# Kernel optimization log

Hardware: AMD Instinct MI355X
Metric: run time of the kernel (lower is better)

Reference implementation:

```python
import jax, jax.numpy as jnp
import numpy as np
import math

N_ENT, N_USR, N_EDGE, C = 100000, 50000, 1000000, 64
N_FACT, N_REL, N_HOPS = 4, 10, 2
KG_HEADS = 2
TEMP = 0.2


def scatter_softmax(scores, seg, num_segments):
    m = jax.ops.segment_max(scores, seg, num_segments=num_segments)
    e = jnp.exp(scores - m[seg])
    s = jax.ops.segment_sum(e, seg, num_segments=num_segments)
    return e / (s[seg] + 1e-16)


def l2norm(x, eps=1e-12):
    n = jnp.linalg.norm(x, axis=-1, keepdims=True)
    return x / jnp.maximum(n, eps)


def setup_inputs() -> dict:
    key = jax.random.key(0)
    ks = jax.random.split(key, 12)
    return {
        "user_emb": jax.random.normal(ks[0], (N_USR, C), jnp.float32) * 0.1,
        "entity_emb": jax.random.normal(ks[1], (N_ENT, C), jnp.float32) * 0.1,
        "latent_emb": jax.random.normal(ks[2], (N_FACT, C), jnp.float32) * 0.1,
        "weight": jax.random.normal(ks[3], (N_REL - 1, C), jnp.float32) * 0.1,
        "disen_weight_att": jax.random.normal(ks[4], (N_FACT, N_REL - 1), jnp.float32) * 0.1,
        "kg_W_r": jax.random.normal(ks[5], (C, C), jnp.float32) * 0.1,
        "ui_vals": jax.random.uniform(ks[6], (N_EDGE,), jnp.float32),
        "edge_index": jax.random.randint(ks[7], (2, N_EDGE), 0, N_ENT, jnp.int64 if jax.config.read('jax_enable_x64') else jnp.int32),
        "edge_type": jax.random.randint(ks[8], (N_EDGE,), 1, N_REL, jnp.int32),
        "ui_rows": jax.random.randint(ks[9], (N_EDGE,), 0, N_USR, jnp.int32),
        "ui_cols": jax.random.randint(ks[10], (N_EDGE,), 0, N_ENT, jnp.int32),
    }


def reference(user_emb, entity_emb, latent_emb, weight, disen_weight_att,
              kg_W_r, ui_vals, edge_index, edge_type, ui_rows, ui_cols):
    head, tail = edge_index[0], edge_index[1]
    d_k = C // KG_HEADS

    # ---- _cul_cor with ind == 'mi' ----
    disen_T = disen_weight_att.T  # [R-1, F]
    nT = disen_T / jnp.linalg.norm(disen_T, axis=1, keepdims=True)
    pos = jnp.sum(nT * nT, axis=1)
    ttl = jnp.sum(disen_T @ disen_weight_att, axis=1)
    cor = -jnp.sum(jnp.log(jnp.exp(pos / TEMP) / jnp.exp(ttl / TEMP)))

    # ---- Invariant_Capture (g_mask=None) ----
    rel_emb = weight[edge_type - 1]          # [E, C]
    head_emb = entity_emb[head]              # [E, C]
    q = (head_emb @ kg_W_r).reshape(-1, KG_HEADS, d_k)
    k = (rel_emb @ kg_W_r).reshape(-1, KG_HEADS, d_k)
    score_r = ((q * k).sum(-1) / math.sqrt(d_k)).mean(-1)  # [E]
    rel_scores = scatter_softmax(score_r, head, N_ENT)
    t_emb = entity_emb[tail]
    r_emb = rel_emb * rel_scores[:, None]
    # bmm of concat(h,r) with concat(t,r) == h.t + r.r
    score_trip = (head_emb * t_emb).sum(-1) + (r_emb * r_emb).sum(-1)
    kg_mask = scatter_softmax(score_trip, head, N_ENT)  # invariant_mask [E]

    # ---- conv_compute: n_hops Aggregator layers, no dropout (eval-determinism) ----
    counts = jnp.clip(jax.ops.segment_sum(jnp.ones_like(kg_mask), head,
                                          num_segments=N_ENT), 1.0)
    disen_w = jax.nn.softmax(disen_weight_att, axis=-1) @ weight  # [F, C]

    ent, usr = entity_emb, user_emb
    ent_res, usr_res = entity_emb, user_emb
    for _ in range(N_HOPS):
        # KG aggregate: scatter_mean over head of masked tail*relation messages
        neigh = ent[tail] * weight[edge_type - 1] * kg_mask[:, None]  # [E, C]
        ent_agg = jax.ops.segment_sum(neigh, head, num_segments=N_ENT) / counts[:, None]
        # user->factor attention on current user embedding
        score = jax.nn.softmax(usr @ latent_emb.T, axis=1)[:, :, None]  # [U, F, 1]
        # sparse user aggregation: interact_mat @ ent
        u_agg = jax.ops.segment_sum(ent[ui_cols] * ui_vals[:, None], ui_rows,
                                    num_segments=N_USR)
        mix = (disen_w[None, :, :] * score).sum(axis=1)  # [U, C]
        u_agg = u_agg * mix + u_agg
        ent = l2norm(ent_agg)
        usr = l2norm(u_agg)
        ent_res = ent_res + ent
        usr_res = usr_res + usr
    return ent_res, usr_res, cor
```

## Files before the change

kernel.cpp:

```cpp
#include <hip/hip_runtime.h>
#include <math.h>

#define N_ENT 100000
#define N_USR 50000
#define N_EDGE 1000000
#define B9 (N_ENT * 9)
#define TEMPC 0.2f
#define KG_BLOCKS (N_ENT / 4)
#define UI_BLOCKS (N_USR / 4)

#define TB_BLOCKS 6250
#define CNT_BLOCKS 489
#define SC_BLOCKS 196
#define REL2_BLOCKS 391

#define BIN_BLOCKS 245
#define NCK 391
#define NCU 196
#define FINEK_BLOCKS NCK
#define FINEU_BLOCKS NCU

#define WLS 68

typedef unsigned short ushort_t;

__device__ __forceinline__ float waveReduceSum(float x) {
#pragma unroll
  for (int d = 32; d > 0; d >>= 1) x += __shfl_xor(x, d);
  return x;
}
__device__ __forceinline__ float waveReduceMax(float x) {
#pragma unroll
  for (int d = 32; d > 0; d >>= 1) x = fmaxf(x, __shfl_xor(x, d));
  return x;
}
__device__ __forceinline__ int waveReduceSumI(int x) {
#pragma unroll
  for (int d = 32; d > 0; d >>= 1) x += __shfl_xor(x, d);
  return x;
}
__device__ __forceinline__ float bf2f(unsigned int u16) {
  union { unsigned int i; float f; } v;
  v.i = u16 << 16;
  return v.f;
}
__device__ __forceinline__ ushort_t f2bf(float f) {
  union { unsigned int i; float f; } v;
  v.f = f;
  unsigned int u = v.i;
  u = (u + 0x7FFFu + ((u >> 16) & 1u)) >> 16;
  return (ushort_t)u;
}
__device__ __forceinline__ int rl(int v, int l) { return __builtin_amdgcn_readlane(v, l); }
__device__ __forceinline__ float rlf(float v, int l) {
  return __int_as_float(__builtin_amdgcn_readlane(__float_as_int(v), l));
}

__device__ __forceinline__ float colRT(float a0, float a1, float a2, float a3,
                                       float a4, float a5, float a6, float a7,
                                       int g, int part) {
#define RED3(x) x += __shfl_xor(x, 8); x += __shfl_xor(x, 16); x += __shfl_xor(x, 32);
  RED3(a0) RED3(a1) RED3(a2) RED3(a3) RED3(a4) RED3(a5) RED3(a6) RED3(a7)
#undef RED3
  float t0 = __shfl(a0, g), t1 = __shfl(a1, g), t2 = __shfl(a2, g), t3 = __shfl(a3, g);
  float t4 = __shfl(a4, g), t5 = __shfl(a5, g), t6 = __shfl(a6, g), t7 = __shfl(a7, g);
  float r = t0;
  r = (part == 1) ? t1 : r;
  r = (part == 2) ? t2 : r;
  r = (part == 3) ? t3 : r;
  r = (part == 4) ? t4 : r;
  r = (part == 5) ? t5 : r;
  r = (part == 6) ? t6 : r;
  r = (part == 7) ? t7 : r;
  return r;
}

__global__ void k_pre(const float* __restrict__ ent0, ushort_t* __restrict__ ent0bf,
                      const int* __restrict__ head, const int* __restrict__ uir,
                      const int* __restrict__ etype,
                      int* __restrict__ cnt_u, int* __restrict__ cnt9,
                      const float* __restrict__ weight, const float* __restrict__ kgW,
                      const float* __restrict__ disen,
                      float* __restrict__ V, float* __restrict__ wsq,
                      float* __restrict__ dw, float* __restrict__ cor_out,
                      const float* __restrict__ user_emb, const float* __restrict__ latent,
                      float4* __restrict__ sc4a) {
  int bid = blockIdx.x;
  if (bid < TB_BLOCKS) {
    int i = bid * 256 + threadIdx.x;
    if (i < N_ENT * 16) {
      float4 v = ((const float4*)ent0)[i];
      ushort4 o;
      o.x = f2bf(v.x); o.y = f2bf(v.y); o.z = f2bf(v.z); o.w = f2bf(v.w);
      ((ushort4*)ent0bf)[i] = o;
    }
  } else if (bid < TB_BLOCKS + CNT_BLOCKS) {
    int i0 = ((bid - TB_BLOCKS) * 256 + threadIdx.x) * 8;
    if (i0 < N_EDGE) {
      int4 ha = *(const int4*)(head + i0), hb = *(const int4*)(head + i0 + 4);
      int4 ea = *(const int4*)(etype + i0), eb = *(const int4*)(etype + i0 + 4);
      int4 ua = *(const int4*)(uir + i0), ub = *(const int4*)(uir + i0 + 4);
      atomicAdd(&cnt9[ha.x * 9 + (ea.x - 1)], 1);
      atomicAdd(&cnt9[ha.y * 9 + (ea.y - 1)], 1);
      atomicAdd(&cnt9[ha.z * 9 + (ea.z - 1)], 1);
      atomicAdd(&cnt9[ha.w * 9 + (ea.w - 1)], 1);
      atomicAdd(&cnt9[hb.x * 9 + (eb.x - 1)], 1);
      atomicAdd(&cnt9[hb.y * 9 + (eb.y - 1)], 1);
      atomicAdd(&cnt9[hb.z * 9 + (eb.z - 1)], 1);
      atomicAdd(&cnt9[hb.w * 9 + (eb.w - 1)], 1);
      atomicAdd(&cnt_u[ua.x], 1);
      atomicAdd(&cnt_u[ua.y], 1);
      atomicAdd(&cnt_u[ua.z], 1);
      atomicAdd(&cnt_u[ua.w], 1);
      atomicAdd(&cnt_u[ub.x], 1);
      atomicAdd(&cnt_u[ub.y], 1);
      atomicAdd(&cnt_u[ub.z], 1);
      atomicAdd(&cnt_u[ub.w], 1);
    }
  } else if (bid == TB_BLOCKS + CNT_BLOCKS) {
    __shared__ float T[9 * 64];
    __shared__ float sm[4 * 9];
    int tid = threadIdx.x;
    for (int e = tid; e < 9 * 64; e += 256) {
      int r = e >> 6, d = e & 63;
      float s = 0.f;
      for (int k = 0; k < 64; ++k) s += kgW[k * 64 + d] * weight[r * 64 + k];
      T[e] = s;
    }
    if (tid < 4) {
      float m = -INFINITY;
      for (int r = 0; r < 9; ++r) m = fmaxf(m, disen[tid * 9 + r]);
      float den = 0.f;
      float ex[9];
      for (int r = 0; r < 9; ++r) { ex[r] = expf(disen[tid * 9 + r] - m); den += ex[r]; }
      for (int r = 0; r < 9; ++r) sm[tid * 9 + r] = ex[r] / den;
    }
    __syncthreads();
    for (int e = tid; e < 9 * 64; e += 256) {
      int r = e >> 6, i = e & 63;
      float s = 0.f;
      for (int d = 0; d < 64; ++d) s += kgW[i * 64 + d] * T[r * 64 + d];
      V[e] = s;
    }
    if (tid < 9) {
      float s = 0.f;
      for (int c = 0; c < 64; ++c) { float w = weight[tid * 64 + c]; s += w * w; }
      wsq[tid] = s;
    }
    for (int e = tid; e < 4 * 64; e += 256) {
      int f = e >> 6, c = e & 63;
      float s = 0.f;
      for (int r = 0; r < 9; ++r) s += sm[f * 9 + r] * weight[r * 64 + c];
      dw[e] = s;
    }
    if (tid == 0) {
      float rowsum[4];
      for (int f = 0; f < 4; ++f) {
        float s = 0.f;
        for (int j = 0; j < 9; ++j) s += disen[f * 9 + j];
        rowsum[f] = s;
      }
      float cor = 0.f;
      for (int i = 0; i < 9; ++i) {
        float n2 = 0.f, ttl = 0.f;
        for (int f = 0; f < 4; ++f) {
          float v = disen[f * 9 + i];
          n2 += v * v;
          ttl += v * rowsum[f];
        }
        float nrm = sqrtf(n2);
        float pos = 0.f;
        for (int f = 0; f < 4; ++f) {
          float v = disen[f * 9 + i] / nrm;
          pos += v * v;
        }
        cor += (ttl - pos) / TEMPC;
      }
      *cor_out = cor;
    }
  } else {
    __shared__ __align__(16) float lat[256];
    if (threadIdx.x < 256) lat[threadIdx.x] = latent[threadIdx.x];
    __syncthreads();
    int u = (bid - TB_BLOCKS - CNT_BLOCKS - 1) * 256 + threadIdx.x;
    if (u >= N_USR) return;
    float a0 = 0.f, a1 = 0.f, a2 = 0.f, a3 = 0.f;
    const float4* row = (const float4*)(user_emb + (size_t)u * 64);
#pragma unroll
    for (int q = 0; q < 16; ++q) {
      float4 v = row[q];
      float4 l0 = *(const float4*)(lat + 0 * 64 + q * 4);
      float4 l1 = *(const float4*)(lat + 1 * 64 + q * 4);
      float4 l2 = *(const float4*)(lat + 2 * 64 + q * 4);
      float4 l3 = *(const float4*)(lat + 3 * 64 + q * 4);
      a0 = fmaf(v.x, l0.x, a0); a0 = fmaf(v.y, l0.y, a0); a0 = fmaf(v.z, l0.z, a0); a0 = fmaf(v.w, l0.w, a0);
      a1 = fmaf(v.x, l1.x, a1); a1 = fmaf(v.y, l1.y, a1); a1 = fmaf(v.z, l1.z, a1); a1 = fmaf(v.w, l1.w, a1);
      a2 = fmaf(v.x, l2.x, a2); a2 = fmaf(v.y, l2.y, a2); a2 = fmaf(v.z, l2.z, a2); a2 = fmaf(v.w, l2.w, a2);
      a3 = fmaf(v.x, l3.x, a3); a3 = fmaf(v.y, l3.y, a3); a3 = fmaf(v.z, l3.z, a3); a3 = fmaf(v.w, l3.w, a3);
    }
    sc4a[u] = make_float4(a0, a1, a2, a3);
  }
}

__global__ void k_scanred(const int* __restrict__ cnt9, const int* __restrict__ cnt_u,
                          int* __restrict__ bsum_h, int* __restrict__ bsum_u, int nbh) {
  int b = blockIdx.x, tid = threadIdx.x;
  int s = 0;
  if (b < nbh) {
    int i0 = b * 1024 + tid * 4;
#pragma unroll
    for (int k = 0; k < 4; ++k)
      if (i0 + k < B9) s += cnt9[i0 + k];
  } else {
    int i0 = (b - nbh) * 1024 + tid * 4;
#pragma unroll
    for (int k = 0; k < 4; ++k)
      if (i0 + k < N_USR) s += cnt_u[i0 + k];
  }
  s = waveReduceSumI(s);
  __shared__ int l[4];
  int lane = tid & 63, wid = tid >> 6;
  if (lane == 0) l[wid] = s;
  __syncthreads();
  if (tid == 0) {
    int v = l[0] + l[1] + l[2] + l[3];
    if (b < nbh) bsum_h[b] = v; else bsum_u[b - nbh] = v;
  }
}

__global__ void __launch_bounds__(1024) k_scan_tops(
    int* bsA, int nA, int* bsB, int nB,
    int* ptrA, int NA, int* ptrB, int NB, int total) {
  __shared__ int wsum[16];
  int tid = threadIdx.x, lane = tid & 63, wid = tid >> 6;
  int v = (tid < nA) ? bsA[tid] : 0;
  int x = v;
#pragma unroll
  for (int d = 1; d < 64; d <<= 1) {
    int y = __shfl_up(x, d);
    if (lane >= d) x += y;
  }
  if (lane == 63) wsum[wid] = x;
  __syncthreads();
  if (tid == 0) {
    int a = 0;
    for (int w = 0; w < 16; ++w) { int t = wsum[w]; wsum[w] = a; a += t; }
  }
  __syncthreads();
  if (tid < nA) bsA[tid] = x - v + wsum[wid];
  if (tid == 0) ptrA[NA] = total;
  __syncthreads();
  int vb = (tid < nB) ? bsB[tid] : 0;
  int xb = vb;
#pragma unroll
  for (int d = 1; d < 64; d <<= 1) {
    int y = __shfl_up(xb, d);
    if (lane >= d) xb += y;
  }
  if (lane == 63) wsum[wid] = xb;
  __syncthreads();
  if (tid == 0) {
    int a = 0;
    for (int w = 0; w < 16; ++w) { int t = wsum[w]; wsum[w] = a; a += t; }
  }
  __syncthreads();
  if (tid < nB) bsB[tid] = xb - vb + wsum[wid];
  if (tid == 0) ptrB[NB] = total;
}

__global__ void k_scanfin(const int* __restrict__ cnt9, const int* __restrict__ cnt_u,
                          const int* __restrict__ bsum_h, const int* __restrict__ bsum_u,
                          int* __restrict__ base9, int* __restrict__ head_ptr,
                          int* __restrict__ ui_ptr,
                          int* __restrict__ coarse_kg_cur, int* __restrict__ coarse_ui_cur,
                          int nbh) {
  int b = blockIdx.x, tid = threadIdx.x;
  bool isH = (b < nbh);
  int bl = isH ? b : b - nbh;
  int n = isH ? B9 : N_USR;
  int i0 = bl * 1024 + tid * 4;
  int s = 0;
  int loc[4];
#pragma unroll
  for (int k = 0; k < 4; ++k) {
    int v = 0;
    if (i0 + k < n) v = isH ? cnt9[i0 + k] : cnt_u[i0 + k];
    loc[k] = s;
    s += v;
  }
  int lane = tid & 63, wid = tid >> 6;
  int x = s;
#pragma unroll
  for (int d = 1; d < 64; d <<= 1) {
    int y = __shfl_up(x, d);
    if (lane >= d) x += y;
  }
  __shared__ int l[4];
  if (lane == 63) l[wid] = x;
  __syncthreads();
  if (tid == 0) {
    int a = 0;
    for (int w = 0; w < 4; ++w) { int t = l[w]; l[w] = a; a += t; }
  }
  __syncthreads();
  int excl = x - s + l[wid] + (isH ? bsum_h[bl] : bsum_u[bl]);
#pragma unroll
  for (int k = 0; k < 4; ++k) {
    int idx = i0 + k;
    if (idx < n) {
      int v = excl + loc[k];
      if (isH) {
        base9[idx] = v;
        int ent = idx / 9;
        if (idx - ent * 9 == 0) {
          head_ptr[ent] = v;
          if ((ent & 255) == 0) coarse_kg_cur[ent >> 8] = v;
        }
      } else {
        ui_ptr[idx] = v;
        if ((idx & 255) == 0) coarse_ui_cur[idx >> 8] = v;
      }
    }
  }
}

__global__ void __launch_bounds__(1024) k_bin(
    const int* __restrict__ head, const int* __restrict__ tail,
    const int* __restrict__ etype,
    const int* __restrict__ uir, const int* __restrict__ uic,
    const float* __restrict__ uival,
    int* __restrict__ coarse_kg_cur, int* __restrict__ coarse_ui_cur,
    unsigned int* __restrict__ stage_kg, int2* __restrict__ stage_ui) {
  __shared__ int histK[NCK], histU[NCU];
  int tid = threadIdx.x;
  for (int i = tid; i < NCK; i += 1024) histK[i] = 0;
  for (int i = tid; i < NCU; i += 1024) histU[i] = 0;
  __syncthreads();
  int i0 = (blockIdx.x * 1024 + tid) * 4;
  bool valid = (i0 < N_EDGE);
  int4 h4, t4v, e4, r4, c4;
  float4 v4;
  int k0 = 0, k1 = 0, k2 = 0, k3 = 0, u0 = 0, u1 = 0, u2 = 0, u3 = 0;
  if (valid) {
    h4 = *(const int4*)(head + i0);
    t4v = *(const int4*)(tail + i0);
    e4 = *(const int4*)(etype + i0);
    r4 = *(const int4*)(uir + i0);
    c4 = *(const int4*)(uic + i0);
    v4 = *(const float4*)(uival + i0);
    k0 = atomicAdd(&histK[h4.x >> 8], 1);
    k1 = atomicAdd(&histK[h4.y >> 8], 1);
    k2 = atomicAdd(&histK[h4.z >> 8], 1);
    k3 = atomicAdd(&histK[h4.w >> 8], 1);
    u0 = atomicAdd(&histU[r4.x >> 8], 1);
    u1 = atomicAdd(&histU[r4.y >> 8], 1);
    u2 = atomicAdd(&histU[r4.z >> 8], 1);
    u3 = atomicAdd(&histU[r4.w >> 8], 1);
  }
  __syncthreads();
  if (tid < NCK) {
    int c = histK[tid];
    histK[tid] = (c > 0) ? atomicAdd(&coarse_kg_cur[tid], c) : 0;
  } else if (tid >= 512 && tid < 512 + NCU) {
    int bu = tid - 512;
    int c = histU[bu];
    histU[bu] = (c > 0) ? atomicAdd(&coarse_ui_cur[bu], c) : 0;
  }
  __syncthreads();
  if (valid) {
    stage_kg[histK[h4.x >> 8] + k0] =
        (unsigned int)(t4v.x | ((e4.x - 1) << 20) | ((h4.x & 255) << 24));
    stage_kg[histK[h4.y >> 8] + k1] =
        (unsigned int)(t4v.y | ((e4.y - 1) << 20) | ((h4.y & 255) << 24));
    stage_kg[histK[h4.z >> 8] + k2] =
        (unsigned int)(t4v.z | ((e4.z - 1) << 20) | ((h4.z & 255) << 24));
    stage_kg[histK[h4.w >> 8] + k3] =
        (unsigned int)(t4v.w | ((e4.w - 1) << 20) | ((h4.w & 255) << 24));
    stage_ui[histU[r4.x >> 8] + u0] = make_int2(c4.x | ((r4.x & 255) << 24), __float_as_int(v4.x));
    stage_ui[histU[r4.y >> 8] + u1] = make_int2(c4.y | ((r4.y & 255) << 24), __float_as_int(v4.y));
    stage_ui[histU[r4.z >> 8] + u2] = make_int2(c4.z | ((r4.z & 255) << 24), __float_as_int(v4.z));
    stage_ui[histU[r4.w >> 8] + u3] = make_int2(c4.w | ((r4.w & 255) << 24), __float_as_int(v4.w));
  }
}

__global__ void k_fine_rel2(const unsigned int* __restrict__ stage_kg,
                            const int2* __restrict__ stage_ui,
                            const int* __restrict__ base9, const int* __restrict__ ui_ptr,
                            int* __restrict__ packed, int2* __restrict__ cv,
                            const ushort_t* __restrict__ ent0bf, const float* __restrict__ V,
                            const float* __restrict__ wsq, const int* __restrict__ cnt9,
                            float* __restrict__ rel2t) {
  int tid = threadIdx.x;
  if (blockIdx.x < FINEK_BLOCKS) {
    int b = blockIdx.x;
    __shared__ int lbase[2304];
    __shared__ int lcnt[2304];
    int gb = (b << 8) * 9;
    for (int i = tid; i < 2304; i += 256) {
      int gi = gb + i;
      lbase[i] = (gi < B9) ? base9[gi] : N_EDGE;
      lcnt[i] = 0;
    }
    __syncthreads();
    int start = base9[gb];
    int end = (b < FINEK_BLOCKS - 1) ? base9[gb + 2304] : N_EDGE;
    for (int i = start + tid; i < end; i += 256) {
      unsigned int w = stage_kg[i];
      int key = (int)((w >> 24) & 255u) * 9 + (int)((w >> 20) & 15u);
      int r = atomicAdd(&lcnt[key], 1);
      packed[lbase[key] + r] = (int)(w & 0xFFFFFFu);
    }
  } else if (blockIdx.x < FINEK_BLOCKS + FINEU_BLOCKS) {
    int b = blockIdx.x - FINEK_BLOCKS;
    __shared__ int lbu[256];
    __shared__ int lcu[256];
    int gb = b << 8;
    lbu[tid] = (gb + tid < N_USR) ? ui_ptr[gb + tid] : N_EDGE;
    lcu[tid] = 0;
    __syncthreads();
    int start = ui_ptr[gb];
    int nxt = gb + 256;
    int end = ui_ptr[(nxt < N_USR) ? nxt : N_USR];
    for (int i = start + tid; i < end; i += 256) {
      int2 d = stage_ui[i];
      int key = (d.x >> 24) & 255;
      int r = atomicAdd(&lcu[key], 1);
      cv[lbu[key] + r] = make_int2(d.x & 0xFFFFFF, d.y);
    }
  } else {
    __shared__ __align__(16) float Vl[576];
    __shared__ float wsql[9];
    for (int i = tid; i < 576; i += 256) Vl[i] = V[i];
    if (tid < 9) wsql[tid] = wsq[tid];
    __syncthreads();
    int ent = (blockIdx.x - FINEK_BLOCKS - FINEU_BLOCKS) * 256 + tid;
    if (ent >= N_ENT) return;
    float a[9] = {0, 0, 0, 0, 0, 0, 0, 0, 0};
    const uint4* row = (const uint4*)(ent0bf + (ent << 6));
#pragma unroll
    for (int q = 0; q < 8; ++q) {
      uint4 b = row[q];
      float ch0 = bf2f(b.x & 0xFFFFu), ch1 = bf2f(b.x >> 16);
      float ch2 = bf2f(b.y & 0xFFFFu), ch3 = bf2f(b.y >> 16);
      float ch4 = bf2f(b.z & 0xFFFFu), ch5 = bf2f(b.z >> 16);
      float ch6 = bf2f(b.w & 0xFFFFu), ch7 = bf2f(b.w >> 16);
#pragma unroll
      for (int r = 0; r < 9; ++r) {
        const float4* vp = (const float4*)(Vl + r * 64 + q * 8);
        float4 v0 = vp[0], v1 = vp[1];
        float t = a[r];
        t = fmaf(ch0, v0.x, t); t = fmaf(ch1, v0.y, t);
        t = fmaf(ch2, v0.z, t); t = fmaf(ch3, v0.w, t);
        t = fmaf(ch4, v1.x, t); t = fmaf(ch5, v1.y, t);
        t = fmaf(ch6, v1.z, t); t = fmaf(ch7, v1.w, t);
        a[r] = t;
      }
    }
    const float inv2s = 0.08838834764831845f;
    int cnt[9];
#pragma unroll
    for (int r = 0; r < 9; ++r) cnt[r] = cnt9[ent * 9 + r];
    float m1 = -INFINITY;
#pragma unroll
    for (int r = 0; r < 9; ++r)
      if (cnt[r] > 0) m1 = fmaxf(m1, a[r] * inv2s);
    if (m1 == -INFINITY) {
#pragma unroll
      for (int r = 0; r < 9; ++r) rel2t[ent * 9 + r] = 0.f;
      return;
    }
    float den1 = 1e-16f;
#pragma unroll
    for (int r = 0; r < 9; ++r)
      if (cnt[r] > 0) den1 += (float)cnt[r] * expf(a[r] * inv2s - m1);
#pragma unroll
    for (int r = 0; r < 9; ++r) {
      float rs = expf(a[r] * inv2s - m1) / den1;
      rel2t[ent * 9 + r] = rs * rs * wsql[r];
    }
  }
}

__device__ __forceinline__ float kg_agg64(int deg, int lane, int pk, float mk,
                                          const ushort_t* __restrict__ srcbf,
                                          const float* __restrict__ wl) {
  float a0 = 0.f, a1 = 0.f, a2 = 0.f, a3 = 0.f;
  int j = 0;
  for (; j + 4 <= deg; j += 4) {
    int p0 = rl(pk, j), p1 = rl(pk, j + 1), p2 = rl(pk, j + 2), p3 = rl(pk, j + 3);
    float k0 = rlf(mk, j), k1 = rlf(mk, j + 1), k2 = rlf(mk, j + 2), k3 = rlf(mk, j + 3);
    float r0 = bf2f(srcbf[((p0 & 0xFFFFF) << 6) + lane]);
    float r1 = bf2f(srcbf[((p1 & 0xFFFFF) << 6) + lane]);
    float r2 = bf2f(srcbf[((p2 & 0xFFFFF) << 6) + lane]);
    float r3 = bf2f(srcbf[((p3 & 0xFFFFF) << 6) + lane]);
    a0 = fmaf(r0 * wl[((p0 >> 20) & 15) * WLS + lane], k0, a0);
    a1 = fmaf(r1 * wl[((p1 >> 20) & 15) * WLS + lane], k1, a1);
    a2 = fmaf(r2 * wl[((p2 >> 20) & 15) * WLS + lane], k2, a2);
    a3 = fmaf(r3 * wl[((p3 >> 20) & 15) * WLS + lane], k3, a3);
  }
  for (; j < deg; ++j) {
    int pj = rl(pk, j);
    float kj = rlf(mk, j);
    a0 = fmaf(bf2f(srcbf[((pj & 0xFFFFF) << 6) + lane]) * wl[((pj >> 20) & 15) * WLS + lane], kj, a0);
  }
  return (a0 + a1) + (a2 + a3);
}

__device__ __forceinline__ void ui_body(int usr, int lane,
                                        const ushort_t* __restrict__ srcbf,
                                        const float4* __restrict__ sc4,
                                        const float* __restrict__ addb,
                                        float* __restrict__ outp, float* __restrict__ nxt,
                                        const int* __restrict__ uptr,
                                        const int2* __restrict__ cv,
                                        const float* __restrict__ dwl,
                                        const float* __restrict__ latl,
                                        float4* __restrict__ sc4out) {
  float4 s4 = sc4[usr];
  float m = fmaxf(fmaxf(s4.x, s4.y), fmaxf(s4.z, s4.w));
  float e0 = expf(s4.x - m), e1 = expf(s4.y - m), e2 = expf(s4.z - m), e3 = expf(s4.w - m);
  float den = e0 + e1 + e2 + e3;
  float mix = (e0 * dwl[lane] + e1 * dwl[64 + lane] + e2 * dwl[128 + lane] + e3 * dwl[192 + lane]) / den;
  int s = uptr[usr], e = uptr[usr + 1];
  int g = lane >> 3, part = lane & 7;
  float a0 = 0.f, a1 = 0.f, a2 = 0.f, a3 = 0.f;
  float a4 = 0.f, a5 = 0.f, a6 = 0.f, a7 = 0.f;
  for (int base = s; base < e; base += 64) {
    int c = min(64, e - base);
    int2 cvl = (lane < c) ? cv[base + lane] : make_int2(0, 0);
    int cl = cvl.x;
    float vl = __int_as_float(cvl.y);
    int nch = (c + 7) >> 3;
#pragma unroll
    for (int cc = 0; cc < 8; ++cc) {
      if (cc < nch) {
        int j = (cc << 3) + g;
        int cj = __shfl(cl, j);
        float vj = __shfl(vl, j);
        uint4 b = *((const uint4*)(srcbf + ((size_t)cj << 6)) + part);
        a0 = fmaf(bf2f(b.x & 0xFFFFu), vj, a0);
        a1 = fmaf(bf2f(b.x >> 16), vj, a1);
        a2 = fmaf(bf2f(b.y & 0xFFFFu), vj, a2);
        a3 = fmaf(bf2f(b.y >> 16), vj, a3);
        a4 = fmaf(bf2f(b.z & 0xFFFFu), vj, a4);
        a5 = fmaf(bf2f(b.z >> 16), vj, a5);
        a6 = fmaf(bf2f(b.w & 0xFFFFu), vj, a6);
        a7 = fmaf(bf2f(b.w >> 16), vj, a7);
      }
    }
  }
  float acc = colRT(a0, a1, a2, a3, a4, a5, a6, a7, g, part);
  float ua = acc * mix + acc;
  float nrm = sqrtf(waveReduceSum(ua * ua));
  float val = ua / fmaxf(nrm, 1e-12f);
  size_t o = (size_t)usr * 64 + lane;
  if (nxt) nxt[o] = val;
  outp[o] = addb[o] + val;
  if (sc4out) {
    float s0 = waveReduceSum(val * latl[lane]);
    float s1 = waveReduceSum(val * latl[64 + lane]);
    float s2 = waveReduceSum(val * latl[128 + lane]);
    float s3 = waveReduceSum(val * latl[192 + lane]);
    if (lane == 0) sc4out[usr] = make_float4(s0, s1, s2, s3);
  }
}

__global__ void k_mask_kg_ui(const float* __restrict__ ent0,
                             const ushort_t* __restrict__ ent0bf,
                             const int* __restrict__ hptr, const int* __restrict__ packed,
                             const float* __restrict__ rel2t,
                             float* __restrict__ mask_s, const float* __restrict__ weight,
                             float* __restrict__ out_ent, ushort_t* __restrict__ ent1bf,
                             const float4* __restrict__ sc4,
                             float* __restrict__ out_usr,
                             float* __restrict__ usr1, const int* __restrict__ uptr,
                             const int2* __restrict__ cv,
                             const float* __restrict__ user_emb, const float* __restrict__ dw,
                             const float* __restrict__ latent, float4* __restrict__ sc4b) {
  int lane = threadIdx.x & 63, wid = threadIdx.x >> 6;
  if (blockIdx.x < KG_BLOCKS) {
    __shared__ __align__(16) float sh_eh[4][64];
    __shared__ __align__(16) float wl[9 * WLS];
    for (int i = threadIdx.x; i < 576; i += 256) wl[(i >> 6) * WLS + (i & 63)] = weight[i];
    int ent = blockIdx.x * 4 + wid;
    int s = hptr[ent], e = hptr[ent + 1];
    float eh = ent0[(size_t)ent * 64 + lane];
    sh_eh[wid][lane] = eh;
    __syncthreads();
    size_t o = (size_t)ent * 64 + lane;
    int deg = e - s;
    if (deg == 0) {
      ent1bf[o] = f2bf(0.f);
      out_ent[o] = eh;
      return;
    }
    if (deg <= 64) {
      int pk = (lane < deg) ? packed[s + lane] : 0;
      int tb = (pk >> 20) & 15;
      float r2sel = rel2t[ent * 9 + ((lane < deg) ? tb : 0)];
      int g = lane >> 3, part = lane & 7;
      const float4* ehq = (const float4*)(sh_eh[wid] + (part << 3));
      float4 ef0 = ehq[0], ef1 = ehq[1];
      int nch = (deg + 7) >> 3;
      float den = 0.f;
      float acc0 = 0.f, acc1 = 0.f, acc2 = 0.f, acc3 = 0.f;
      float acc4 = 0.f, acc5 = 0.f, acc6 = 0.f, acc7 = 0.f;
      float ws8[8];
#pragma unroll
      for (int cc = 0; cc < 8; ++cc) {
        ws8[cc] = 0.f;
        if (cc < nch) {
          int j = (cc << 3) + g;
          int pkj = __shfl(pk, j);
          uint4 b = *((const uint4*)(ent0bf + ((size_t)(pkj & 0xFFFFF) << 6)) + part);
          float r0 = bf2f(b.x & 0xFFFFu), r1 = bf2f(b.x >> 16);
          float r2 = bf2f(b.y & 0xFFFFu), r3 = bf2f(b.y >> 16);
          float r4 = bf2f(b.z & 0xFFFFu), r5 = bf2f(b.z >> 16);
          float r6 = bf2f(b.w & 0xFFFFu), r7 = bf2f(b.w >> 16);
          float s0 = r0 * ef0.x, s1 = r2 * ef0.z, s2 = r4 * ef1.x, s3 = r6 * ef1.z;
          s0 = fmaf(r1, ef0.y, s0); s1 = fmaf(r3, ef0.w, s1);
          s2 = fmaf(r5, ef1.y, s2); s3 = fmaf(r7, ef1.w, s3);
          float sv = (s0 + s1) + (s2 + s3);
          sv += __shfl_xor(sv, 1);
          sv += __shfl_xor(sv, 2);
          sv += __shfl_xor(sv, 4);
          float r2j = __shfl(r2sel, j);
          float w = (j < deg) ? expf(sv + r2j) : 0.f;
          ws8[cc] = w;
          den += w;
          const float4* wp = (const float4*)(wl + ((pkj >> 20) & 15) * WLS + (part << 3));
          float4 w0 = wp[0], w1 = wp[1];
// ... 29 lines not shown
    } else {
      float m2l = -INFINITY;
      for (int base = s; base < e; base += 64) {
        int c = min(64, e - base);
        int pk = (lane < c) ? packed[base + lane] : 0;
        int tb = (pk >> 20) & 15;
        float r2 = rel2t[ent * 9 + ((lane < c) ? tb : 0)];
        int tl = pk & 0xFFFFF;
        const uint4* row = (const uint4*)(ent0bf + (tl << 6));
        const float* ehp = sh_eh[wid];
        float d = 0.f;
#pragma unroll
        for (int q = 0; q < 8; ++q) {
          uint4 a = row[q];
          d += bf2f(a.x & 0xFFFF) * ehp[q * 8 + 0] + bf2f(a.x >> 16) * ehp[q * 8 + 1];
          d += bf2f(a.y & 0xFFFF) * ehp[q * 8 + 2] + bf2f(a.y >> 16) * ehp[q * 8 + 3];
          d += bf2f(a.z & 0xFFFF) * ehp[q * 8 + 4] + bf2f(a.z >> 16) * ehp[q * 8 + 5];
          d += bf2f(a.w & 0xFFFF) * ehp[q * 8 + 6] + bf2f(a.w >> 16) * ehp[q * 8 + 7];
        }
        float trip = d + r2;
        if (lane < c) {
          mask_s[base + lane] = trip;
          m2l = fmaxf(m2l, trip);
        }
      }
      float m2 = waveReduceMax(m2l);
      float denl = 0.f;
      for (int base = s; base < e; base += 64) {
        int c = min(64, e - base);
        denl += (lane < c) ? expf(mask_s[base + lane] - m2) : 0.f;
      }
      float den2 = waveReduceSum(denl) + 1e-16f;
      float acc = 0.f;
      for (int base = s; base < e; base += 64) {
        int c = min(64, e - base);
        int pk = (lane < c) ? packed[base + lane] : 0;
        float mk = 0.f;
        if (lane < c) {
          mk = expf(mask_s[base + lane] - m2) / den2;
          mask_s[base + lane] = mk;
        }
        acc += kg_agg64(c, lane, pk, mk, ent0bf, wl);
      }
      float agg = acc / (float)deg;
      float nrm = sqrtf(waveReduceSum(agg * agg));
      float val = agg / fmaxf(nrm, 1e-12f);
      ent1bf[o] = f2bf(val);
      out_ent[o] = eh + val;
    }
  } else {
    __shared__ float dwl[256];
    __shared__ float latl[256];
    if (threadIdx.x < 256) {
      dwl[threadIdx.x] = dw[threadIdx.x];
      latl[threadIdx.x] = latent[threadIdx.x];
    }
    __syncthreads();
    int usr = (blockIdx.x - KG_BLOCKS) * 4 + wid;
    ui_body(usr, lane, ent0bf, sc4, user_emb, out_usr, usr1,
            uptr, cv, dwl, latl, sc4b);
  }
}

__global__ void k_hop2(const ushort_t* __restrict__ srcbf,
                       float* __restrict__ out_ent,
                       const int* __restrict__ hptr, const int* __restrict__ packed,
                       const float* __restrict__ mask_s, const float* __restrict__ weight,
                       const float* __restrict__ usr1, float* __restrict__ out_usr,
                       const int* __restrict__ uptr, const int2* __restrict__ cv,
                       const float4* __restrict__ sc4,
                       const float* __restrict__ dw) {
  int lane = threadIdx.x & 63, wid = threadIdx.x >> 6;
  if (blockIdx.x < KG_BLOCKS) {
    __shared__ __align__(16) float wl[9 * WLS];
    for (int i = threadIdx.x; i < 576; i += 256) wl[(i >> 6) * WLS + (i & 63)] = weight[i];
    __syncthreads();
    int ent = blockIdx.x * 4 + wid;
    int s = hptr[ent], e = hptr[ent + 1];
    int g = lane >> 3, part = lane & 7;
    float a0 = 0.f, a1 = 0.f, a2 = 0.f, a3 = 0.f;
    float a4 = 0.f, a5 = 0.f, a6 = 0.f, a7 = 0.f;
    for (int base = s; base < e; base += 64) {
      int c = min(64, e - base);
      int pk = (lane < c) ? packed[base + lane] : 0;
      float mk = (lane < c) ? mask_s[base + lane] : 0.f;
      int nch = (c + 7) >> 3;
#pragma unroll
      for (int cc = 0; cc < 8; ++cc) {
        if (cc < nch) {
          int j = (cc << 3) + g;
          int pkj = __shfl(pk, j);
          float mkj = __shfl(mk, j);
          uint4 b = *((const uint4*)(srcbf + ((size_t)(pkj & 0xFFFFF) << 6)) + part);
          float r0 = bf2f(b.x & 0xFFFFu), r1 = bf2f(b.x >> 16);
          float r2 = bf2f(b.y & 0xFFFFu), r3 = bf2f(b.y >> 16);
          float r4 = bf2f(b.z & 0xFFFFu), r5 = bf2f(b.z >> 16);
          float r6 = bf2f(b.w & 0xFFFFu), r7 = bf2f(b.w >> 16);
          const float4* wp = (const float4*)(wl + ((pkj >> 20) & 15) * WLS + (part << 3));
          float4 w0 = wp[0], w1 = wp[1];
          a0 = fmaf(mkj * r0, w0.x, a0);
          a1 = fmaf(mkj * r1, w0.y, a1);
          a2 = fmaf(mkj * r2, w0.z, a2);
          a3 = fmaf(mkj * r3, w0.w, a3);
          a4 = fmaf(mkj * r4, w1.x, a4);
          a5 = fmaf(mkj * r5, w1.y, a5);
          a6 = fmaf(mkj * r6, w1.z, a6);
          a7 = fmaf(mkj * r7, w1.w, a7);
        }
      }
    }
    float aggv = colRT(a0, a1, a2, a3, a4, a5, a6, a7, g, part);
    float n = (float)(e - s);
    float agg = aggv / fmaxf(n, 1.0f);
    float nrm = sqrtf(waveReduceSum(agg * agg));
    float val = agg / fmaxf(nrm, 1e-12f);
    size_t o = (size_t)ent * 64 + lane;
    out_ent[o] = out_ent[o] + val;
  } else {
    __shared__ float dwl[256];
    if (threadIdx.x < 256) dwl[threadIdx.x] = dw[threadIdx.x];
    __syncthreads();
    int usr = (blockIdx.x - KG_BLOCKS) * 4 + wid;
    ui_body(usr, lane, srcbf, sc4, out_usr, out_usr, nullptr,
            uptr, cv, dwl, nullptr, nullptr);
  }
}

extern "C" void kernel_launch(void* const* d_in, const int* in_sizes, int n_in,
                              void* d_out, int out_size, void* d_ws, size_t ws_size,
                              hipStream_t stream) {
  const float* user_emb = (const float*)d_in[0];
  const float* entity_emb = (const float*)d_in[1];
  const float* latent = (const float*)d_in[2];
  const float* weight = (const float*)d_in[3];
  const float* disen = (const float*)d_in[4];
  const float* kgW = (const float*)d_in[5];
  const float* ui_vals = (const float*)d_in[6];
  const int* edge_index = (const int*)d_in[7];
  const int* edge_type = (const int*)d_in[8];
  const int* ui_rows = (const int*)d_in[9];
  const int* ui_cols = (const int*)d_in[10];
  const int* head = edge_index;
  const int* tail = edge_index + N_EDGE;

  char* ws = (char*)d_ws;
  size_t o = 0;
  auto alloc = [&](size_t bytes) -> char* {
    char* p = ws + o;
    o += (bytes + 255) & ~(size_t)255;
    return p;
  };
  int* head_ptr = (int*)alloc((N_ENT + 1) * 4);
  int* ui_ptr = (int*)alloc((N_USR + 1) * 4);
  int* cnt_u = (int*)alloc((size_t)N_USR * 4);
  int* bsum_h = (int*)alloc(1024 * 4);
  int* bsum_u = (int*)alloc(64 * 4);
  int* packed = (int*)alloc((size_t)N_EDGE * 4);
  int2* cv = (int2*)alloc((size_t)N_EDGE * 8);
  float* mask_s = (float*)alloc((size_t)N_EDGE * 4);
  ushort_t* ent0bf = (ushort_t*)alloc((size_t)N_ENT * 64 * 2);
  ushort_t* ent1bf = (ushort_t*)alloc((size_t)N_ENT * 64 * 2);
  float* usr1 = (float*)alloc((size_t)N_USR * 64 * 4);
  int* cnt9 = (int*)alloc((size_t)B9 * 4);
  int* base9 = (int*)alloc((size_t)B9 * 4);
  unsigned int* stage_kg = (unsigned int*)alloc((size_t)N_EDGE * 4);
  int2* stage_ui = (int2*)alloc((size_t)N_EDGE * 8);
  int* coarse_kg_cur = (int*)alloc(NCK * 4);
  int* coarse_ui_cur = (int*)alloc(NCU * 4);
  float* rel2t = (float*)alloc((size_t)N_ENT * 9 * 4);
  float4* sc4a = (float4*)alloc((size_t)N_USR * 16);
  float4* sc4b = (float4*)alloc((size_t)N_USR * 16);
  float* V = (float*)alloc(9 * 64 * 4);
  float* wsq = (float*)alloc(16 * 4);
  float* dw = (float*)alloc(4 * 64 * 4);
  if (o > ws_size) return;

  float* out_ent = (float*)d_out;
  float* out_usr = out_ent + (size_t)N_ENT * 64;
  float* out_cor = out_ent + (size_t)N_ENT * 64 + (size_t)N_USR * 64;

  hipMemsetAsync(cnt_u, 0, (size_t)N_USR * 4, stream);
  hipMemsetAsync(cnt9, 0, (size_t)B9 * 4, stream);

  k_pre<<<TB_BLOCKS + CNT_BLOCKS + 1 + SC_BLOCKS, 256, 0, stream>>>(
      entity_emb, ent0bf, head, ui_rows, edge_type, cnt_u, cnt9,
      weight, kgW, disen, V, wsq, dw, out_cor, user_emb, latent, sc4a);

  int nbh = (B9 + 1023) / 1024;
  int nbu = (N_USR + 1023) / 1024;
  k_scanred<<<nbh + nbu, 256, 0, stream>>>(cnt9, cnt_u, bsum_h, bsum_u, nbh);
  k_scan_tops<<<1, 1024, 0, stream>>>(bsum_h, nbh, bsum_u, nbu, head_ptr, N_ENT, ui_ptr, N_USR, N_EDGE);
  k_scanfin<<<nbh + nbu, 256, 0, stream>>>(cnt9, cnt_u, bsum_h, bsum_u,
                                           base9, head_ptr, ui_ptr,
                                           coarse_kg_cur, coarse_ui_cur, nbh);
  k_bin<<<BIN_BLOCKS, 1024, 0, stream>>>(
      head, tail, edge_type, ui_rows, ui_cols, ui_vals,
      coarse_kg_cur, coarse_ui_cur, stage_kg, stage_ui);
  k_fine_rel2<<<FINEK_BLOCKS + FINEU_BLOCKS + REL2_BLOCKS, 256, 0, stream>>>(
      stage_kg, stage_ui, base9, ui_ptr, packed, cv,
      ent0bf, V, wsq, cnt9, rel2t);

  k_mask_kg_ui<<<KG_BLOCKS + UI_BLOCKS, 256, 0, stream>>>(
      entity_emb, ent0bf, head_ptr, packed, rel2t, mask_s, weight,
      out_ent, ent1bf, sc4a, out_usr, usr1, ui_ptr, cv, user_emb, dw, latent, sc4b);

  k_hop2<<<KG_BLOCKS + UI_BLOCKS, 256, 0, stream>>>(
      ent1bf, out_ent, head_ptr, packed, mask_s, weight,
      usr1, out_usr, ui_ptr, cv, sc4b, dw);
}
```

Baseline: 478.4 us.

## Replace fine-grained global counting and scan with coarse shared-memory histograms

Edge counting now builds per-block shared-memory histograms over coarse 256-entity or 256-user buckets and flushes them with a few global atomics, replacing 16 global atomics per thread into large per-(entity,relation) and per-user count arrays. The three-kernel multi-level scan becomes a single small coarse scan. Fine per-entity/relation offsets are now derived inside the fine binning blocks with a local counting pass and block scan, and the rel2 softmax computation is folded into those blocks using the local counts. This removes large memsets, global atomic traffic and two launches, at the cost of reading the staged edges twice in the fine pass.

```diff
diff --git a/kernel.cpp b/kernel.cpp
--- a/kernel.cpp
+++ b/kernel.cpp
@@ -4,7 +4,6 @@
 #define N_ENT 100000
 #define N_USR 50000
 #define N_EDGE 1000000
-#define B9 (N_ENT * 9)
 #define TEMPC 0.2f
 #define KG_BLOCKS (N_ENT / 4)
 #define UI_BLOCKS (N_USR / 4)
@@ -12,7 +11,6 @@
 #define TB_BLOCKS 6250
 #define CNT_BLOCKS 489
 #define SC_BLOCKS 196
-#define REL2_BLOCKS 391
 
 #define BIN_BLOCKS 245
 #define NCK 391
@@ -77,8 +75,7 @@
 
 __global__ void k_pre(const float* __restrict__ ent0, ushort_t* __restrict__ ent0bf,
                       const int* __restrict__ head, const int* __restrict__ uir,
-                      const int* __restrict__ etype,
-                      int* __restrict__ cnt_u, int* __restrict__ cnt9,
+                      int* __restrict__ ccnt_kg, int* __restrict__ ccnt_ui,
                       const float* __restrict__ weight, const float* __restrict__ kgW,
                       const float* __restrict__ disen,
                       float* __restrict__ V, float* __restrict__ wsq,
@@ -95,28 +92,37 @@
       ((ushort4*)ent0bf)[i] = o;
     }
   } else if (bid < TB_BLOCKS + CNT_BLOCKS) {
-    int i0 = ((bid - TB_BLOCKS) * 256 + threadIdx.x) * 8;
+    __shared__ int histK[NCK], histU[NCU];
+    int tid = threadIdx.x;
+    for (int i = tid; i < NCK; i += 256) histK[i] = 0;
+    for (int i = tid; i < NCU; i += 256) histU[i] = 0;
+    __syncthreads();
+    int i0 = ((bid - TB_BLOCKS) * 256 + tid) * 8;
     if (i0 < N_EDGE) {
       int4 ha = *(const int4*)(head + i0), hb = *(const int4*)(head + i0 + 4);
-      int4 ea = *(const int4*)(etype + i0), eb = *(const int4*)(etype + i0 + 4);
       int4 ua = *(const int4*)(uir + i0), ub = *(const int4*)(uir + i0 + 4);
-      atomicAdd(&cnt9[ha.x * 9 + (ea.x - 1)], 1);
-      atomicAdd(&cnt9[ha.y * 9 + (ea.y - 1)], 1);
-      atomicAdd(&cnt9[ha.z * 9 + (ea.z - 1)], 1);
-      atomicAdd(&cnt9[ha.w * 9 + (ea.w - 1)], 1);
-      atomicAdd(&cnt9[hb.x * 9 + (eb.x - 1)], 1);
-      atomicAdd(&cnt9[hb.y * 9 + (eb.y - 1)], 1);
-      atomicAdd(&cnt9[hb.z * 9 + (eb.z - 1)], 1);
-      atomicAdd(&cnt9[hb.w * 9 + (eb.w - 1)], 1);
-      atomicAdd(&cnt_u[ua.x], 1);
-      atomicAdd(&cnt_u[ua.y], 1);
-      atomicAdd(&cnt_u[ua.z], 1);
-      atomicAdd(&cnt_u[ua.w], 1);
-      atomicAdd(&cnt_u[ub.x], 1);
-      atomicAdd(&cnt_u[ub.y], 1);
-      atomicAdd(&cnt_u[ub.z], 1);
-      atomicAdd(&cnt_u[ub.w], 1);
-    }
+      atomicAdd(&histK[ha.x >> 8], 1);
+      atomicAdd(&histK[ha.y >> 8], 1);
+      atomicAdd(&histK[ha.z >> 8], 1);
+      atomicAdd(&histK[ha.w >> 8], 1);
+      atomicAdd(&histK[hb.x >> 8], 1);
+      atomicAdd(&histK[hb.y >> 8], 1);
+      atomicAdd(&histK[hb.z >> 8], 1);
+      atomicAdd(&histK[hb.w >> 8], 1);
+      atomicAdd(&histU[ua.x >> 8], 1);
+      atomicAdd(&histU[ua.y >> 8], 1);
+      atomicAdd(&histU[ua.z >> 8], 1);
+      atomicAdd(&histU[ua.w >> 8], 1);
+      atomicAdd(&histU[ub.x >> 8], 1);
+      atomicAdd(&histU[ub.y >> 8], 1);
+      atomicAdd(&histU[ub.z >> 8], 1);
+      atomicAdd(&histU[ub.w >> 8], 1);
+    }
+    __syncthreads();
+    for (int i = tid; i < NCK; i += 256)
+      if (histK[i] > 0) atomicAdd(&ccnt_kg[i], histK[i]);
+    for (int i = tid; i < NCU; i += 256)
+      if (histU[i] > 0) atomicAdd(&ccnt_ui[i], histU[i]);
   } else if (bid == TB_BLOCKS + CNT_BLOCKS) {
     __shared__ float T[9 * 64];
     __shared__ float sm[4 * 9];
@@ -202,38 +208,14 @@
   }
 }
 
-__global__ void k_scanred(const int* __restrict__ cnt9, const int* __restrict__ cnt_u,
-                          int* __restrict__ bsum_h, int* __restrict__ bsum_u, int nbh) {
-  int b = blockIdx.x, tid = threadIdx.x;
-  int s = 0;
-  if (b < nbh) {
-    int i0 = b * 1024 + tid * 4;
-#pragma unroll
-    for (int k = 0; k < 4; ++k)
-      if (i0 + k < B9) s += cnt9[i0 + k];
-  } else {
-    int i0 = (b - nbh) * 1024 + tid * 4;
-#pragma unroll
-    for (int k = 0; k < 4; ++k)
-      if (i0 + k < N_USR) s += cnt_u[i0 + k];
-  }
-  s = waveReduceSumI(s);
-  __shared__ int l[4];
-  int lane = tid & 63, wid = tid >> 6;
-  if (lane == 0) l[wid] = s;
-  __syncthreads();
-  if (tid == 0) {
-    int v = l[0] + l[1] + l[2] + l[3];
-    if (b < nbh) bsum_h[b] = v; else bsum_u[b - nbh] = v;
-  }
-}
-
-__global__ void __launch_bounds__(1024) k_scan_tops(
-    int* bsA, int nA, int* bsB, int nB,
-    int* ptrA, int NA, int* ptrB, int NB, int total) {
+__global__ void __launch_bounds__(1024) k_scan_coarse(
+    const int* __restrict__ ccnt_kg, const int* __restrict__ ccnt_ui,
+    int* __restrict__ cbase_kg, int* __restrict__ cbase_ui,
+    int* __restrict__ cur_kg, int* __restrict__ cur_ui,
+    int* __restrict__ head_ptr, int* __restrict__ ui_ptr) {
   __shared__ int wsum[16];
   int tid = threadIdx.x, lane = tid & 63, wid = tid >> 6;
-  int v = (tid < nA) ? bsA[tid] : 0;
+  int v = (tid < NCK) ? ccnt_kg[tid] : 0;
   int x = v;
 #pragma unroll
   for (int d = 1; d < 64; d <<= 1) {
@@ -247,81 +229,27 @@
     for (int w = 0; w < 16; ++w) { int t = wsum[w]; wsum[w] = a; a += t; }
   }
   __syncthreads();
-  if (tid < nA) bsA[tid] = x - v + wsum[wid];
-  if (tid == 0) ptrA[NA] = total;
+  int base = x - v + wsum[wid];
+  if (tid < NCK) { cbase_kg[tid] = base; cur_kg[tid] = base; }
+  if (tid == 0) { cbase_kg[NCK] = N_EDGE; head_ptr[N_ENT] = N_EDGE; }
   __syncthreads();
-  int vb = (tid < nB) ? bsB[tid] : 0;
-  int xb = vb;
+  int vu = (tid < NCU) ? ccnt_ui[tid] : 0;
+  int xu = vu;
 #pragma unroll
   for (int d = 1; d < 64; d <<= 1) {
-    int y = __shfl_up(xb, d);
-    if (lane >= d) xb += y;
-  }
-  if (lane == 63) wsum[wid] = xb;
+    int y = __shfl_up(xu, d);
+    if (lane >= d) xu += y;
+  }
+  if (lane == 63) wsum[wid] = xu;
   __syncthreads();
   if (tid == 0) {
     int a = 0;
     for (int w = 0; w < 16; ++w) { int t = wsum[w]; wsum[w] = a; a += t; }
   }
   __syncthreads();
-  if (tid < nB) bsB[tid] = xb - vb + wsum[wid];
-  if (tid == 0) ptrB[NB] = total;
-}
-
-__global__ void k_scanfin(const int* __restrict__ cnt9, const int* __restrict__ cnt_u,
-                          const int* __restrict__ bsum_h, const int* __restrict__ bsum_u,
-                          int* __restrict__ base9, int* __restrict__ head_ptr,
-                          int* __restrict__ ui_ptr,
-                          int* __restrict__ coarse_kg_cur, int* __restrict__ coarse_ui_cur,
-                          int nbh) {
-  int b = blockIdx.x, tid = threadIdx.x;
-  bool isH = (b < nbh);
-  int bl = isH ? b : b - nbh;
-  int n = isH ? B9 : N_USR;
-  int i0 = bl * 1024 + tid * 4;
-  int s = 0;
-  int loc[4];
-#pragma unroll
-  for (int k = 0; k < 4; ++k) {
-    int v = 0;
-    if (i0 + k < n) v = isH ? cnt9[i0 + k] : cnt_u[i0 + k];
-    loc[k] = s;
-    s += v;
-  }
-  int lane = tid & 63, wid = tid >> 6;
-  int x = s;
-#pragma unroll
-  for (int d = 1; d < 64; d <<= 1) {
-    int y = __shfl_up(x, d);
-    if (lane >= d) x += y;
-  }
-  __shared__ int l[4];
-  if (lane == 63) l[wid] = x;
-  __syncthreads();
-  if (tid == 0) {
-    int a = 0;
-    for (int w = 0; w < 4; ++w) { int t = l[w]; l[w] = a; a += t; }
-  }
-  __syncthreads();
-  int excl = x - s + l[wid] + (isH ? bsum_h[bl] : bsum_u[bl]);
-#pragma unroll
-  for (int k = 0; k < 4; ++k) {
-    int idx = i0 + k;
-    if (idx < n) {
-      int v = excl + loc[k];
-      if (isH) {
-        base9[idx] = v;
-        int ent = idx / 9;
-        if (idx - ent * 9 == 0) {
-          head_ptr[ent] = v;
-          if ((ent & 255) == 0) coarse_kg_cur[ent >> 8] = v;
-        }
-      } else {
-        ui_ptr[idx] = v;
-        if ((idx & 255) == 0) coarse_ui_cur[idx >> 8] = v;
-      }
-    }
-  }
+  int bu = xu - vu + wsum[wid];
+  if (tid < NCU) { cbase_ui[tid] = bu; cur_ui[tid] = bu; }
+  if (tid == 0) { cbase_ui[NCU] = N_EDGE; ui_ptr[N_USR] = N_EDGE; }
 }
 
 __global__ void __launch_bounds__(1024) k_bin(
@@ -385,98 +313,156 @@
 
 __global__ void k_fine_rel2(const unsigned int* __restrict__ stage_kg,
                             const int2* __restrict__ stage_ui,
-                            const int* __restrict__ base9, const int* __restrict__ ui_ptr,
+                            const int* __restrict__ cbase_kg, const int* __restrict__ cbase_ui,
                             int* __restrict__ packed, int2* __restrict__ cv,
+                            int* __restrict__ head_ptr, int* __restrict__ ui_ptr,
                             const ushort_t* __restrict__ ent0bf, const float* __restrict__ V,
-                            const float* __restrict__ wsq, const int* __restrict__ cnt9,
-                            float* __restrict__ rel2t) {
+                            const float* __restrict__ wsq, float* __restrict__ rel2t) {
   int tid = threadIdx.x;
+  int lane = tid & 63, wid = tid >> 6;
   if (blockIdx.x < FINEK_BLOCKS) {
     int b = blockIdx.x;
     __shared__ int lbase[2304];
     __shared__ int lcnt[2304];
-    int gb = (b << 8) * 9;
-    for (int i = tid; i < 2304; i += 256) {
-      int gi = gb + i;
-      lbase[i] = (gi < B9) ? base9[gi] : N_EDGE;
-      lcnt[i] = 0;
-    }
-    __syncthreads();
-    int start = base9[gb];
-    int end = (b < FINEK_BLOCKS - 1) ? base9[gb + 2304] : N_EDGE;
-    for (int i = start + tid; i < end; i += 256) {
+    __shared__ __align__(16) float Vl[576];
+    __shared__ float wsql[9];
+    __shared__ int woff[4];
+    for (int i = tid; i < 2304; i += 256) lcnt[i] = 0;
+    for (int i = tid; i < 576; i += 256) Vl[i] = V[i];
+    if (tid < 9) wsql[tid] = wsq[tid];
+    int cs = cbase_kg[b], ce = cbase_kg[b + 1];
+    int gb = b << 8;
+    int ne = min(256, N_ENT - gb);
+    __syncthreads();
+    for (int i = cs + tid; i < ce; i += 256) {
+      unsigned int w = stage_kg[i];
+      int key = (int)((w >> 24) & 255u) * 9 + (int)((w >> 20) & 15u);
+      atomicAdd(&lcnt[key], 1);
+    }
+    __syncthreads();
+    int pre9[9];
+    int deg = 0;
+    if (tid < ne) {
+#pragma unroll
+      for (int r = 0; r < 9; ++r) { pre9[r] = deg; deg += lcnt[tid * 9 + r]; }
+    }
+    int x = deg;
+#pragma unroll
+    for (int d = 1; d < 64; d <<= 1) {
+      int y = __shfl_up(x, d);
+      if (lane >= d) x += y;
+    }
+    if (lane == 63) woff[wid] = x;
+    __syncthreads();
+    if (tid == 0) {
+      int a = 0;
+      for (int w2 = 0; w2 < 4; ++w2) { int t = woff[w2]; woff[w2] = a; a += t; }
+    }
+    __syncthreads();
+    int ebase = cs + (x - deg) + woff[wid];
+    if (tid < ne) {
+      head_ptr[gb + tid] = ebase;
+#pragma unroll
+      for (int r = 0; r < 9; ++r) lbase[tid * 9 + r] = ebase + pre9[r];
+    }
+    __syncthreads();
+    for (int i = tid; i < 2304; i += 256) lcnt[i] = 0;
+    __syncthreads();
+    for (int i = cs + tid; i < ce; i += 256) {
       unsigned int w = stage_kg[i];
       int key = (int)((w >> 24) & 255u) * 9 + (int)((w >> 20) & 15u);
       int r = atomicAdd(&lcnt[key], 1);
       packed[lbase[key] + r] = (int)(w & 0xFFFFFFu);
     }
-  } else if (blockIdx.x < FINEK_BLOCKS + FINEU_BLOCKS) {
+    __syncthreads();
+    if (tid < ne) {
+      int ent = gb + tid;
+      float a[9] = {0, 0, 0, 0, 0, 0, 0, 0, 0};
+      const uint4* row = (const uint4*)(ent0bf + ((size_t)ent << 6));
+#pragma unroll
+      for (int q = 0; q < 8; ++q) {
+        uint4 bq = row[q];
+        float ch0 = bf2f(bq.x & 0xFFFFu), ch1 = bf2f(bq.x >> 16);
+        float ch2 = bf2f(bq.y & 0xFFFFu), ch3 = bf2f(bq.y >> 16);
+        float ch4 = bf2f(bq.z & 0xFFFFu), ch5 = bf2f(bq.z >> 16);
+        float ch6 = bf2f(bq.w & 0xFFFFu), ch7 = bf2f(bq.w >> 16);
+#pragma unroll
+        for (int r = 0; r < 9; ++r) {
+          const float4* vp = (const float4*)(Vl + r * 64 + q * 8);
+          float4 v0 = vp[0], v1 = vp[1];
+          float t = a[r];
+          t = fmaf(ch0, v0.x, t); t = fmaf(ch1, v0.y, t);
+          t = fmaf(ch2, v0.z, t); t = fmaf(ch3, v0.w, t);
+          t = fmaf(ch4, v1.x, t); t = fmaf(ch5, v1.y, t);
+          t = fmaf(ch6, v1.z, t); t = fmaf(ch7, v1.w, t);
+          a[r] = t;
+        }
+      }
+      const float inv2s = 0.08838834764831845f;
+      int cnt[9];
+#pragma unroll
+      for (int r = 0; r < 9; ++r) cnt[r] = lcnt[tid * 9 + r];
+      float m1 = -INFINITY;
+#pragma unroll
+      for (int r = 0; r < 9; ++r)
+        if (cnt[r] > 0) m1 = fmaxf(m1, a[r] * inv2s);
+      if (m1 == -INFINITY) {
+#pragma unroll
+        for (int r = 0; r < 9; ++r) rel2t[ent * 9 + r] = 0.f;
+      } else {
+        float den1 = 1e-16f;
+#pragma unroll
+        for (int r = 0; r < 9; ++r)
+          if (cnt[r] > 0) den1 += (float)cnt[r] * expf(a[r] * inv2s - m1);
+#pragma unroll
+        for (int r = 0; r < 9; ++r) {
+          float rs = expf(a[r] * inv2s - m1) / den1;
+          rel2t[ent * 9 + r] = rs * rs * wsql[r];
+        }
+      }
+    }
+  } else {
     int b = blockIdx.x - FINEK_BLOCKS;
     __shared__ int lbu[256];
     __shared__ int lcu[256];
+    __shared__ int woff2[4];
+    lcu[tid] = 0;
+    int cs = cbase_ui[b], ce = cbase_ui[b + 1];
     int gb = b << 8;
-    lbu[tid] = (gb + tid < N_USR) ? ui_ptr[gb + tid] : N_EDGE;
+    int nu = min(256, N_USR - gb);
+    __syncthreads();
+    for (int i = cs + tid; i < ce; i += 256) {
+      int2 d = stage_ui[i];
+      atomicAdd(&lcu[(d.x >> 24) & 255], 1);
+    }
+    __syncthreads();
+    int deg = (tid < nu) ? lcu[tid] : 0;
+    int x = deg;
+#pragma unroll
+    for (int d = 1; d < 64; d <<= 1) {
+      int y = __shfl_up(x, d);
+      if (lane >= d) x += y;
+    }
+    if (lane == 63) woff2[wid] = x;
+    __syncthreads();
+    if (tid == 0) {
+      int a = 0;
+      for (int w2 = 0; w2 < 4; ++w2) { int t = woff2[w2]; woff2[w2] = a; a += t; }
+    }
+    __syncthreads();
+    int ubase = cs + (x - deg) + woff2[wid];
+    __syncthreads();
+    if (tid < nu) {
+      ui_ptr[gb + tid] = ubase;
+      lbu[tid] = ubase;
+    }
     lcu[tid] = 0;
     __syncthreads();
-    int start = ui_ptr[gb];
-    int nxt = gb + 256;
-    int end = ui_ptr[(nxt < N_USR) ? nxt : N_USR];
-    for (int i = start + tid; i < end; i += 256) {
+    for (int i = cs + tid; i < ce; i += 256) {
       int2 d = stage_ui[i];
       int key = (d.x >> 24) & 255;
       int r = atomicAdd(&lcu[key], 1);
       cv[lbu[key] + r] = make_int2(d.x & 0xFFFFFF, d.y);
-    }
-  } else {
-    __shared__ __align__(16) float Vl[576];
-    __shared__ float wsql[9];
-    for (int i = tid; i < 576; i += 256) Vl[i] = V[i];
-    if (tid < 9) wsql[tid] = wsq[tid];
-    __syncthreads();
-    int ent = (blockIdx.x - FINEK_BLOCKS - FINEU_BLOCKS) * 256 + tid;
-    if (ent >= N_ENT) return;
-    float a[9] = {0, 0, 0, 0, 0, 0, 0, 0, 0};
-    const uint4* row = (const uint4*)(ent0bf + (ent << 6));
-#pragma unroll
-    for (int q = 0; q < 8; ++q) {
-      uint4 b = row[q];
-      float ch0 = bf2f(b.x & 0xFFFFu), ch1 = bf2f(b.x >> 16);
-      float ch2 = bf2f(b.y & 0xFFFFu), ch3 = bf2f(b.y >> 16);
-      float ch4 = bf2f(b.z & 0xFFFFu), ch5 = bf2f(b.z >> 16);
-      float ch6 = bf2f(b.w & 0xFFFFu), ch7 = bf2f(b.w >> 16);
-#pragma unroll
-      for (int r = 0; r < 9; ++r) {
-        const float4* vp = (const float4*)(Vl + r * 64 + q * 8);
-        float4 v0 = vp[0], v1 = vp[1];
-        float t = a[r];
-        t = fmaf(ch0, v0.x, t); t = fmaf(ch1, v0.y, t);
-        t = fmaf(ch2, v0.z, t); t = fmaf(ch3, v0.w, t);
-        t = fmaf(ch4, v1.x, t); t = fmaf(ch5, v1.y, t);
-        t = fmaf(ch6, v1.z, t); t = fmaf(ch7, v1.w, t);
-        a[r] = t;
-      }
-    }
-    const float inv2s = 0.08838834764831845f;
-    int cnt[9];
-#pragma unroll
-    for (int r = 0; r < 9; ++r) cnt[r] = cnt9[ent * 9 + r];
-    float m1 = -INFINITY;
-#pragma unroll
-    for (int r = 0; r < 9; ++r)
-      if (cnt[r] > 0) m1 = fmaxf(m1, a[r] * inv2s);
-    if (m1 == -INFINITY) {
-#pragma unroll
-      for (int r = 0; r < 9; ++r) rel2t[ent * 9 + r] = 0.f;
-      return;
-    }
-    float den1 = 1e-16f;
-#pragma unroll
-    for (int r = 0; r < 9; ++r)
-      if (cnt[r] > 0) den1 += (float)cnt[r] * expf(a[r] * inv2s - m1);
-#pragma unroll
-    for (int r = 0; r < 9; ++r) {
-      float rs = expf(a[r] * inv2s - m1) / den1;
-      rel2t[ent * 9 + r] = rs * rs * wsql[r];
     }
   }
 }
@@ -812,21 +798,21 @@
   };
   int* head_ptr = (int*)alloc((N_ENT + 1) * 4);
   int* ui_ptr = (int*)alloc((N_USR + 1) * 4);
-  int* cnt_u = (int*)alloc((size_t)N_USR * 4);
-  int* bsum_h = (int*)alloc(1024 * 4);
-  int* bsum_u = (int*)alloc(64 * 4);
   int* packed = (int*)alloc((size_t)N_EDGE * 4);
   int2* cv = (int2*)alloc((size_t)N_EDGE * 8);
   float* mask_s = (float*)alloc((size_t)N_EDGE * 4);
   ushort_t* ent0bf = (ushort_t*)alloc((size_t)N_ENT * 64 * 2);
   ushort_t* ent1bf = (ushort_t*)alloc((size_t)N_ENT * 64 * 2);
   float* usr1 = (float*)alloc((size_t)N_USR * 64 * 4);
-  int* cnt9 = (int*)alloc((size_t)B9 * 4);
-  int* base9 = (int*)alloc((size_t)B9 * 4);
   unsigned int* stage_kg = (unsigned int*)alloc((size_t)N_EDGE * 4);
   int2* stage_ui = (int2*)alloc((size_t)N_EDGE * 8);
-  int* coarse_kg_cur = (int*)alloc(NCK * 4);
-  int* coarse_ui_cur = (int*)alloc(NCU * 4);
+  int* ccnt = (int*)alloc((NCK + NCU) * 4);
+  int* ccnt_kg = ccnt;
+  int* ccnt_ui = ccnt + NCK;
+  int* cbase_kg = (int*)alloc((NCK + 1) * 4);
+  int* cbase_ui = (int*)alloc((NCU + 1) * 4);
+  int* cur_kg = (int*)alloc(NCK * 4);
+  int* cur_ui = (int*)alloc(NCU * 4);
   float* rel2t = (float*)alloc((size_t)N_ENT * 9 * 4);
   float4* sc4a = (float4*)alloc((size_t)N_USR * 16);
   float4* sc4b = (float4*)alloc((size_t)N_USR * 16);
@@ -839,26 +825,22 @@
   float* out_usr = out_ent + (size_t)N_ENT * 64;
   float* out_cor = out_ent + (size_t)N_ENT * 64 + (size_t)N_USR * 64;
 
-  hipMemsetAsync(cnt_u, 0, (size_t)N_USR * 4, stream);
-  hipMemsetAsync(cnt9, 0, (size_t)B9 * 4, stream);
+  hipMemsetAsync(ccnt, 0, (NCK + NCU) * 4, stream);
 
   k_pre<<<TB_BLOCKS + CNT_BLOCKS + 1 + SC_BLOCKS, 256, 0, stream>>>(
-      entity_emb, ent0bf, head, ui_rows, edge_type, cnt_u, cnt9,
+      entity_emb, ent0bf, head, ui_rows, ccnt_kg, ccnt_ui,
       weight, kgW, disen, V, wsq, dw, out_cor, user_emb, latent, sc4a);
 
-  int nbh = (B9 + 1023) / 1024;
-  int nbu = (N_USR + 1023) / 1024;
-  k_scanred<<<nbh + nbu, 256, 0, stream>>>(cnt9, cnt_u, bsum_h, bsum_u, nbh);
-  k_scan_tops<<<1, 1024, 0, stream>>>(bsum_h, nbh, bsum_u, nbu, head_ptr, N_ENT, ui_ptr, N_USR, N_EDGE);
-  k_scanfin<<<nbh + nbu, 256, 0, stream>>>(cnt9, cnt_u, bsum_h, bsum_u,
-                                           base9, head_ptr, ui_ptr,
-                                           coarse_kg_cur, coarse_ui_cur, nbh);
+  k_scan_coarse<<<1, 1024, 0, stream>>>(ccnt_kg, ccnt_ui, cbase_kg, cbase_ui,
+                                        cur_kg, cur_ui, head_ptr, ui_ptr);
+
   k_bin<<<BIN_BLOCKS, 1024, 0, stream>>>(
       head, tail, edge_type, ui_rows, ui_cols, ui_vals,
-      coarse_kg_cur, coarse_ui_cur, stage_kg, stage_ui);
-  k_fine_rel2<<<FINEK_BLOCKS + FINEU_BLOCKS + REL2_BLOCKS, 256, 0, stream>>>(
-      stage_kg, stage_ui, base9, ui_ptr, packed, cv,
-      ent0bf, V, wsq, cnt9, rel2t);
+      cur_kg, cur_ui, stage_kg, stage_ui);
+
+  k_fine_rel2<<<FINEK_BLOCKS + FINEU_BLOCKS, 256, 0, stream>>>(
+      stage_kg, stage_ui, cbase_kg, cbase_ui, packed, cv,
+      head_ptr, ui_ptr, ent0bf, V, wsq, rel2t);
 
   k_mask_kg_ui<<<KG_BLOCKS + UI_BLOCKS, 256, 0, stream>>>(
       entity_emb, ent0bf, head_ptr, packed, rel2t, mask_s, weight,
```

Measured after the change: 405.4 us. 15.2% less time.
